# Performance work log

Hardware: AMD Instinct MI355X
Metric: run time of the kernel (lower is better)

## Reference

```python
import jax, jax.numpy as jnp
import numpy as np

EPS = 1e-5

def _ln(x, gamma, beta):
    mu = jnp.mean(x, axis=-1, keepdims=True)
    var = jnp.mean(jnp.square(x - mu), axis=-1, keepdims=True)
    return (x - mu) * jax.lax.rsqrt(var + EPS) * gamma + beta

def _linear(x, w, b):
    # torch nn.Linear convention: w is [out, in]
    return jnp.einsum('...i,oi->...o', x, w) + b

def setup_inputs() -> dict:
    key = jax.random.key(0)
    B, L, C = 1, 384, 128
    ks = jax.random.split(key, 16)
    s = 1.0 / np.sqrt(C)
    inp = {
        'pair_feat': jax.random.normal(ks[0], (B, L, L, C), dtype=jnp.float32),
        'res_mask': jnp.ones((B, L), dtype=jnp.float32),
        # left_proj: Linear + LayerNorm
        'lp_w': jax.random.uniform(ks[1], (C, C), jnp.float32, -s, s),
        'lp_b': jnp.zeros((C,), jnp.float32),
        'lp_g': jnp.ones((C,), jnp.float32),
        'lp_beta': jnp.zeros((C,), jnp.float32),
        # right_proj: Linear + LayerNorm
        'rp_w': jax.random.uniform(ks[2], (C, C), jnp.float32, -s, s),
        'rp_b': jnp.zeros((C,), jnp.float32),
        'rp_g': jnp.ones((C,), jnp.float32),
        'rp_beta': jnp.zeros((C,), jnp.float32),
        # gates: Linear (then sigmoid)
        'lg_w': jax.random.uniform(ks[3], (C, C), jnp.float32, -s, s),
        'lg_b': jnp.zeros((C,), jnp.float32),
        'rg_w': jax.random.uniform(ks[4], (C, C), jnp.float32, -s, s),
        'rg_b': jnp.zeros((C,), jnp.float32),
        'og_w': jax.random.uniform(ks[5], (C, C), jnp.float32, -s, s),
        'og_b': jnp.zeros((C,), jnp.float32),
        # out_layer: LayerNorm + Linear
        'ol_g': jnp.ones((C,), jnp.float32),
        'ol_beta': jnp.zeros((C,), jnp.float32),
        'ow': jax.random.uniform(ks[6], (C, C), jnp.float32, -s, s),
        'ob': jnp.zeros((C,), jnp.float32),
    }
    return inp

def reference(pair_feat, res_mask, lp_w, lp_b, lp_g, lp_beta,
              rp_w, rp_b, rp_g, rp_beta, lg_w, lg_b, rg_w, rg_b,
              og_w, og_b, ol_g, ol_beta, ow, ob):
    # op_type == 'outgoing': einsum 'bikc,bjkc->bijc'
    proj_left = _ln(_linear(pair_feat, lp_w, lp_b), lp_g, lp_beta)
    proj_right = _ln(_linear(pair_feat, rp_w, rp_b), rp_g, rp_beta)
    mask2d = (res_mask[:, :, None] * res_mask[:, None, :])[..., None]  # [B,L,L,1]
    proj_left = proj_left * mask2d
    proj_right = proj_right * mask2d
    gate_left = jax.nn.sigmoid(_linear(pair_feat, lg_w, lg_b))
    gate_right = jax.nn.sigmoid(_linear(pair_feat, rg_w, rg_b))
    proj_left = proj_left * gate_left
    proj_right = proj_right * gate_right
    out = jnp.einsum('bikc,bjkc->bijc', proj_left, proj_right)
    out = _linear(_ln(out, ol_g, ol_beta), ow, ob)
    gate = jax.nn.sigmoid(_linear(pair_feat, og_w, og_b))
    return out * gate
```

## Files before the change

kernel.cpp:

```cpp
#include <hip/hip_runtime.h>

typedef __bf16 bf16x8 __attribute__((ext_vector_type(8)));
typedef __bf16 bf16x4 __attribute__((ext_vector_type(4)));
typedef float  f32x4  __attribute__((ext_vector_type(4)));
typedef float  f32x2  __attribute__((ext_vector_type(2)));
typedef int    int4v  __attribute__((ext_vector_type(4)));

#define LL    384
#define CC    128
#define NROW  (LL * LL)

#define MFMA16(a, b, c) __builtin_amdgcn_mfma_f32_16x16x32_bf16((a), (b), (c), 0, 0, 0)

__device__ __forceinline__ bf16x8 cvt8(const float* p) {
    f32x4 a = *reinterpret_cast<const f32x4*>(p);
    f32x4 b = *reinterpret_cast<const f32x4*>(p + 4);
    bf16x8 r;
    r[0] = (__bf16)a[0]; r[1] = (__bf16)a[1]; r[2] = (__bf16)a[2]; r[3] = (__bf16)a[3];
    r[4] = (__bf16)b[0]; r[5] = (__bf16)b[1]; r[6] = (__bf16)b[2]; r[7] = (__bf16)b[3];
    return r;
}
__device__ __forceinline__ bf16x8 ld_ws(const __bf16* p) {
    return __builtin_bit_cast(bf16x8, *reinterpret_cast<const int4v*>(p));
}
__device__ __forceinline__ float sigmf(float x) { return 1.f / (1.f + __expf(-x)); }

__device__ __forceinline__ void gl16(const __bf16* g, __bf16* l) {
    __builtin_amdgcn_global_load_lds(
        (const __attribute__((address_space(1))) unsigned int*)g,
        (__attribute__((address_space(3))) unsigned int*)l,
        16, 0, 0);
}

__device__ __forceinline__ void stage_weight(const float* __restrict__ w,
                                             __bf16* dst, int tid) {
    const int c   = tid >> 1;
    const int k0  = (tid & 1) * 64;
    const int nt  = c >> 4;
    const int n16 = c & 15;
    #pragma unroll
    for (int u = 0; u < 8; ++u) {
        const int k    = k0 + u * 8;
        const int ks   = k >> 5;
        const int quad = (k >> 3) & 3;
        bf16x8 v = cvt8(w + c * CC + k);
        *reinterpret_cast<int4v*>(dst + ((ks * 8 + nt) * 64 + quad * 16 + n16) * 8) =
            __builtin_bit_cast(int4v, v);
    }
}
__device__ __forceinline__ bf16x8 wfrag(const __bf16* base, int ks, int nt, int lane) {
    return ld_ws(base + ((ks * 8 + nt) * 64 + lane) * 8);
}

__global__ __launch_bounds__(256, 2) void k_proj(
    const float* __restrict__ pf, const float* __restrict__ rmask,
    const float* __restrict__ lp_w, const float* __restrict__ lp_b,
    const float* __restrict__ lp_g, const float* __restrict__ lp_be,
    const float* __restrict__ rp_w, const float* __restrict__ rp_b,
    const float* __restrict__ rp_g, const float* __restrict__ rp_be,
    const float* __restrict__ lg_w, const float* __restrict__ lg_b,
    const float* __restrict__ rg_w, const float* __restrict__ rg_b,
    __bf16* __restrict__ pl_c, __bf16* __restrict__ pr_c)
{
    __shared__ __bf16 wl[2 * 16384];

    const int tid  = threadIdx.x;
    const int wave = tid >> 6, lane = tid & 63;
    const int n16  = lane & 15, quad = lane >> 4;
    const int rowblock = blockIdx.x * 128 + wave * 32;

    bf16x8 xf[2][4];
    #pragma unroll
    for (int rg = 0; rg < 2; ++rg) {
        const int r_a = rowblock + rg * 16 + n16;
        #pragma unroll
        for (int ks = 0; ks < 4; ++ks)
            xf[rg][ks] = cvt8(pf + (size_t)r_a * CC + ks * 32 + quad * 8);
    }

    float mrow[2][4];
    #pragma unroll
    for (int rg = 0; rg < 2; ++rg) {
        const int rd   = rowblock + rg * 16 + quad * 4;
        const int i_id = rd / LL;
        const int k_id = rd - i_id * LL;
        float mi = rmask[i_id];
        #pragma unroll
        for (int g = 0; g < 4; ++g) mrow[rg][g] = mi * rmask[k_id + g];
    }

    auto phase = [&](const float* gw, const float* gb,
                     const float* pw, const float* pb,
                     const float* gamma, const float* beta,
                     __bf16* dst) {
        stage_weight(gw, wl, tid);
        stage_weight(pw, wl + 16384, tid);
        __syncthreads();

        f32x4 acc[2][8];
        #pragma unroll
        for (int rg = 0; rg < 2; ++rg)
            #pragma unroll
            for (int nt = 0; nt < 8; ++nt) acc[rg][nt] = f32x4{0.f, 0.f, 0.f, 0.f};
        #pragma unroll
        for (int ks = 0; ks < 4; ++ks)
            #pragma unroll
            for (int nt = 0; nt < 8; ++nt) {
                bf16x8 wf = wfrag(wl, ks, nt, lane);
                #pragma unroll
                for (int rg = 0; rg < 2; ++rg)
                    acc[rg][nt] = MFMA16(xf[rg][ks], wf, acc[rg][nt]);
            }
        bf16x4 sg[2][8];
        #pragma unroll
        for (int rg = 0; rg < 2; ++rg)
            #pragma unroll
            for (int nt = 0; nt < 8; ++nt) {
                float bias = gb[nt * 16 + n16];
                #pragma unroll
                for (int g = 0; g < 4; ++g)
                    sg[rg][nt][g] = (__bf16)sigmf(acc[rg][nt][g] + bias);
            }
        #pragma unroll
        for (int rg = 0; rg < 2; ++rg)
            #pragma unroll
            for (int nt = 0; nt < 8; ++nt) acc[rg][nt] = f32x4{0.f, 0.f, 0.f, 0.f};
        #pragma unroll
        for (int ks = 0; ks < 4; ++ks)
            #pragma unroll
            for (int nt = 0; nt < 8; ++nt) {
                bf16x8 wf = wfrag(wl + 16384, ks, nt, lane);
                #pragma unroll
                for (int rg = 0; rg < 2; ++rg)
                    acc[rg][nt] = MFMA16(xf[rg][ks], wf, acc[rg][nt]);
            }
        #pragma unroll
        for (int rg = 0; rg < 2; ++rg) {
            #pragma unroll
            for (int nt = 0; nt < 8; ++nt) {
                float bias = pb[nt * 16 + n16];
                #pragma unroll
                for (int g = 0; g < 4; ++g) acc[rg][nt][g] += bias;
            }
            float s[4] = {0.f,0.f,0.f,0.f}, ss[4] = {0.f,0.f,0.f,0.f};
            #pragma unroll
            for (int nt = 0; nt < 8; ++nt)
                #pragma unroll
                for (int g = 0; g < 4; ++g) { float v = acc[rg][nt][g]; s[g] += v; ss[g] += v * v; }
            #pragma unroll
            for (int m = 1; m < 16; m <<= 1)
                #pragma unroll
                for (int g = 0; g < 4; ++g) {
                    s[g]  += __shfl_xor(s[g],  m, 64);
                    ss[g] += __shfl_xor(ss[g], m, 64);
                }
            float mean[4], rstd[4];
            #pragma unroll
            for (int g = 0; g < 4; ++g) {
                mean[g] = s[g] * (1.f / 128.f);
                float var = ss[g] * (1.f / 128.f) - mean[g] * mean[g];
                rstd[g] = rsqrtf(fmaxf(var, 0.f) + 1e-5f);
            }
            const int rd = rowblock + rg * 16 + quad * 4;
            #pragma unroll
            for (int nt = 0; nt < 8; ++nt) {
                const int c = nt * 16 + n16;
                float ga = gamma[c], be = beta[c];
                bf16x4 o;
                #pragma unroll
                for (int g = 0; g < 4; ++g) {
                    float v = (acc[rg][nt][g] - mean[g]) * rstd[g] * ga + be;
                    v *= mrow[rg][g] * (float)sg[rg][nt][g];
                    o[g] = (__bf16)v;
                }
                *reinterpret_cast<bf16x4*>(dst + (size_t)c * NROW + rd) = o;
            }
        }
        __syncthreads();
    };

    phase(lg_w, lg_b, lp_w, lp_b, lp_g, lp_be, pl_c);
    phase(rg_w, rg_b, rp_w, rp_b, rp_g, rp_be, pr_c);
}

__global__ __launch_bounds__(256, 3) void k_einsum_tile(
    const __bf16* __restrict__ pl_c, const __bf16* __restrict__ pr_c,
    float* __restrict__ T)
{
    __shared__ __bf16 sA[2][512 * 8];
    __shared__ __bf16 sB[2][512 * 8];

    const int bid  = blockIdx.x;
    const int wgid = (bid & 7) * 144 + (bid >> 3);
    const int ch   = wgid / 9;
    const int tile = wgid - ch * 9;
    const int i0   = (tile / 3) * 128;
    const int j0   = (tile % 3) * 128;

    const int tid  = threadIdx.x;
    const int w    = tid >> 6, lane = tid & 63;
    const int n16  = lane & 15, quad = lane >> 4;
    const int wr   = w >> 1, wc = w & 1;

    const __bf16* Pc = pl_c + (size_t)ch * NROW;
    const __bf16* Qc = pr_c + (size_t)ch * NROW;

    const __bf16* ga[2];
    const __bf16* gb[2];
    #pragma unroll
    for (int u = 0; u < 2; ++u) {
        const int row = (w * 2 + u) * 16 + n16;
        ga[u] = Pc + (size_t)(i0 + row) * LL + quad * 8;
        gb[u] = Qc + (size_t)(j0 + row) * LL + quad * 8;
    }

    f32x4 acc[4][4];
    #pragma unroll
    for (int m = 0; m < 4; ++m)
        #pragma unroll
        for (int n = 0; n < 4; ++n) acc[m][n] = f32x4{0.f, 0.f, 0.f, 0.f};

    auto STAGE = [&](int buf, int k0) {
        #pragma unroll
        for (int u = 0; u < 2; ++u) {
            __bf16* la = &sA[buf][(size_t)((w * 2 + u) * 64) * 8];
            __bf16* lb = &sB[buf][(size_t)((w * 2 + u) * 64) * 8];
            gl16(ga[u] + k0, la);
            gl16(gb[u] + k0, lb);
        }
    };

    STAGE(0, 0);
    __syncthreads();

    #pragma unroll
    for (int t = 0; t < 12; ++t) {
        if (t < 11) STAGE((t + 1) & 1, (t + 1) * 32);
        const __bf16* Ab = sA[t & 1];
        const __bf16* Bb = sB[t & 1];
        bf16x8 af[4], bf[4];
        #pragma unroll
        for (int m = 0; m < 4; ++m) af[m] = ld_ws(Ab + ((size_t)((wr * 4 + m) * 64 + lane)) * 8);
        #pragma unroll
        for (int n = 0; n < 4; ++n) bf[n] = ld_ws(Bb + ((size_t)((wc * 4 + n) * 64 + lane)) * 8);
        #pragma unroll
        for (int m = 0; m < 4; ++m)
            #pragma unroll
            for (int n = 0; n < 4; ++n)
                acc[m][n] = MFMA16(af[m], bf[n], acc[m][n]);
        __syncthreads();
    }

    float* Tc = T + (size_t)ch * NROW;
    #pragma unroll
    for (int m = 0; m < 4; ++m) {
        const int i = i0 + wr * 64 + m * 16 + quad * 4;
        #pragma unroll
        for (int n = 0; n < 4; ++n) {
            const int j = j0 + wc * 64 + n * 16 + n16;
            #pragma unroll
            for (int g = 0; g < 4; ++g)
                Tc[(size_t)(i + g) * LL + j] = acc[m][n][g];
        }
    }
}

__global__ __launch_bounds__(256, 2) void k_final_cm(
    float* __restrict__ out, const float* __restrict__ T,
    const float* __restrict__ pf,
    const float* __restrict__ ol_g, const float* __restrict__ ol_be,
    const float* __restrict__ ow,   const float* __restrict__ ob,
    const float* __restrict__ og_w, const float* __restrict__ og_b)
{
    __shared__ __bf16 wl[2 * 16384];
    const int tid  = threadIdx.x;
    const int wave = tid >> 6, lane = tid & 63;
    const int n16  = lane & 15, quad = lane >> 4;
    const int rowblock = blockIdx.x * 128 + wave * 32;

    stage_weight(ow,   wl,         tid);
    stage_weight(og_w, wl + 16384, tid);
    __syncthreads();

    #pragma unroll
    for (int rg = 0; rg < 2; ++rg) {
        const int r = rowblock + rg * 16 + n16;

        f32x4 tf[8];
        bf16x8 pff[4];
        #pragma unroll
        for (int ks = 0; ks < 4; ++ks) {
            #pragma unroll
            for (int q = 0; q < 4; ++q) {
                tf[2 * ks][q]     = T[(size_t)(ks * 32 + quad * 8 + q)     * NROW + r];
                tf[2 * ks + 1][q] = T[(size_t)(ks * 32 + quad * 8 + 4 + q) * NROW + r];
            }
            pff[ks] = cvt8(pf + (size_t)r * CC + ks * 32 + quad * 8);
        }

        float s = 0.f, ss = 0.f;
        #pragma unroll
        for (int h = 0; h < 8; ++h)
            #pragma unroll
            for (int q = 0; q < 4; ++q) { float f = tf[h][q]; s += f; ss += f * f; }
        s += __shfl_xor(s, 16, 64);  ss += __shfl_xor(ss, 16, 64);
        s += __shfl_xor(s, 32, 64);  ss += __shfl_xor(ss, 32, 64);
        const float mean = s * (1.f / 128.f);
        const float rstd = rsqrtf(fmaxf(ss * (1.f / 128.f) - mean * mean, 0.f) + 1e-5f);

        bf16x8 xn[4];
        #pragma unroll
        for (int ks = 0; ks < 4; ++ks) {
            const int cb = ks * 32 + quad * 8;
            f32x4 g0 = *reinterpret_cast<const f32x4*>(ol_g + cb);
            f32x4 g1 = *reinterpret_cast<const f32x4*>(ol_g + cb + 4);
            f32x4 b0 = *reinterpret_cast<const f32x4*>(ol_be + cb);
            f32x4 b1 = *reinterpret_cast<const f32x4*>(ol_be + cb + 4);
            bf16x8 rv;
            #pragma unroll
            for (int q = 0; q < 4; ++q) {
                rv[q]     = (__bf16)((tf[2 * ks][q]     - mean) * rstd * g0[q] + b0[q]);
                rv[4 + q] = (__bf16)((tf[2 * ks + 1][q] - mean) * rstd * g1[q] + b1[q]);
            }
            xn[ks] = rv;
        }

        f32x4 ao[8], ag[8];
        #pragma unroll
        for (int mt = 0; mt < 8; ++mt) { ao[mt] = f32x4{0.f,0.f,0.f,0.f}; ag[mt] = f32x4{0.f,0.f,0.f,0.f}; }
        #pragma unroll
        for (int ks = 0; ks < 4; ++ks)
            #pragma unroll
            for (int mt = 0; mt < 8; ++mt) {
                bf16x8 awf = wfrag(wl,         ks, mt, lane);
                bf16x8 gwf = wfrag(wl + 16384, ks, mt, lane);
                ao[mt] = MFMA16(awf, xn[ks],  ao[mt]);
                ag[mt] = MFMA16(gwf, pff[ks], ag[mt]);
            }

        #pragma unroll
        for (int mt = 0; mt < 8; ++mt) {
            const int c0 = mt * 16 + quad * 4;
            f32x4 bb = *reinterpret_cast<const f32x4*>(ob + c0);
            f32x4 gb = *reinterpret_cast<const f32x4*>(og_b + c0);
            f32x4 o;
            #pragma unroll
            for (int g = 0; g < 4; ++g) {
                float gate = sigmf(ag[mt][g] + gb[g]);
                o[g] = (ao[mt][g] + bb[g]) * gate;
            }
            *reinterpret_cast<f32x4*>(out + (size_t)r * CC + c0) = o;
        }
    }
}

__global__ __launch_bounds__(256, 2) void k_einsum_direct(
    const __bf16* __restrict__ pl_c, const __bf16* __restrict__ pr_c,
    float* __restrict__ out)
{
    const int tid  = threadIdx.x;
    const int wave = tid >> 6, lane = tid & 63;
    const int n16  = lane & 15, quad = lane >> 4;
    const int i0   = blockIdx.x * 64;
    const int jw   = blockIdx.y * 64 + wave * 16;
    const int c0   = blockIdx.z * 8;

    size_t off_i[4];
    #pragma unroll
    for (int t = 0; t < 4; ++t)
        off_i[t] = (size_t)(i0 + t * 16 + n16) * LL + quad * 8;
    const size_t off_j = (size_t)(jw + n16) * LL + quad * 8;

    f32x4 acc[8][4];
    #pragma unroll
    for (int c = 0; c < 8; ++c)
        #pragma unroll
        for (int t = 0; t < 4; ++t) acc[c][t] = f32x4{0.f, 0.f, 0.f, 0.f};

    #pragma unroll
    for (int c = 0; c < 8; ++c) {
        const __bf16* Pb = pl_c + (size_t)(c0 + c) * NROW;
        const __bf16* Qb = pr_c + (size_t)(c0 + c) * NROW + off_j;
        #pragma unroll
        for (int kt = 0; kt < 12; ++kt) {
            bf16x8 fj = ld_ws(Qb + kt * 32);
            #pragma unroll
            for (int t = 0; t < 4; ++t) {
                bf16x8 fi = ld_ws(Pb + off_i[t] + kt * 32);
                acc[c][t] = MFMA16(fi, fj, acc[c][t]);
            }
        }
    }

    #pragma unroll
    for (int t = 0; t < 4; ++t)
        #pragma unroll
        for (int g = 0; g < 4; ++g) {
            const int i = i0 + t * 16 + quad * 4 + g;
            float* dst = out + ((size_t)i * LL + jw + n16) * CC + c0;
            f32x4 lo, hi;
            #pragma unroll
            for (int q = 0; q < 4; ++q) { lo[q] = acc[q][t][g]; hi[q] = acc[4 + q][t][g]; }
            *reinterpret_cast<f32x4*>(dst)     = lo;
            *reinterpret_cast<f32x4*>(dst + 4) = hi;
        }
}

__global__ __launch_bounds__(256, 2) void k_final_ip(
    float* out, const float* __restrict__ pf,
    const float* __restrict__ ol_g, const float* __restrict__ ol_be,
    const float* __restrict__ ow,   const float* __restrict__ ob,
    const float* __restrict__ og_w, const float* __restrict__ og_b)
{
    __shared__ __bf16 wl[2 * 16384];
    const int tid  = threadIdx.x;
    const int wave = tid >> 6, lane = tid & 63;
    const int n16  = lane & 15, quad = lane >> 4;
    const int rowblock = blockIdx.x * 128 + wave * 32;

    stage_weight(ow,   wl,         tid);
    stage_weight(og_w, wl + 16384, tid);
    __syncthreads();

    #pragma unroll
    for (int rg = 0; rg < 2; ++rg) {
        const int r = rowblock + rg * 16 + n16;

        f32x4 tf[8];
        bf16x8 pff[4];
        #pragma unroll
        for (int ks = 0; ks < 4; ++ks) {
            const float* tp = out + (size_t)r * CC + ks * 32 + quad * 8;
            tf[2 * ks]     = *reinterpret_cast<const f32x4*>(tp);
            tf[2 * ks + 1] = *reinterpret_cast<const f32x4*>(tp + 4);
            pff[ks] = cvt8(pf + (size_t)r * CC + ks * 32 + quad * 8);
        }

        float s = 0.f, ss = 0.f;
        #pragma unroll
        for (int h = 0; h < 8; ++h)
            #pragma unroll
            for (int q = 0; q < 4; ++q) { float f = tf[h][q]; s += f; ss += f * f; }
        s += __shfl_xor(s, 16, 64);  ss += __shfl_xor(ss, 16, 64);
        s += __shfl_xor(s, 32, 64);  ss += __shfl_xor(ss, 32, 64);
        const float mean = s * (1.f / 128.f);
        const float rstd = rsqrtf(fmaxf(ss * (1.f / 128.f) - mean * mean, 0.f) + 1e-5f);

        bf16x8 xn[4];
        #pragma unroll
        for (int ks = 0; ks < 4; ++ks) {
            const int cb = ks * 32 + quad * 8;
            f32x4 g0 = *reinterpret_cast<const f32x4*>(ol_g + cb);
            f32x4 g1 = *reinterpret_cast<const f32x4*>(ol_g + cb + 4);
            f32x4 b0 = *reinterpret_cast<const f32x4*>(ol_be + cb);
            f32x4 b1 = *reinterpret_cast<const f32x4*>(ol_be + cb + 4);
            bf16x8 rv;
            #pragma unroll
            for (int q = 0; q < 4; ++q) {
                rv[q]     = (__bf16)((tf[2 * ks][q]     - mean) * rstd * g0[q] + b0[q]);
                rv[4 + q] = (__bf16)((tf[2 * ks + 1][q] - mean) * rstd * g1[q] + b1[q]);
            }
            xn[ks] = rv;
        }

        f32x4 ao[8], ag[8];
        #pragma unroll
        for (int mt = 0; mt < 8; ++mt) { ao[mt] = f32x4{0.f,0.f,0.f,0.f}; ag[mt] = f32x4{0.f,0.f,0.f,0.f}; }
        #pragma unroll
        for (int ks = 0; ks < 4; ++ks)
            #pragma unroll
            for (int mt = 0; mt < 8; ++mt) {
                bf16x8 awf = wfrag(wl,         ks, mt, lane);
                bf16x8 gwf = wfrag(wl + 16384, ks, mt, lane);
                ao[mt] = MFMA16(awf, xn[ks],  ao[mt]);
                ag[mt] = MFMA16(gwf, pff[ks], ag[mt]);
            }

        #pragma unroll
        for (int mt = 0; mt < 8; ++mt) {
            const int c0 = mt * 16 + quad * 4;
            f32x4 bb = *reinterpret_cast<const f32x4*>(ob + c0);
            f32x4 gb = *reinterpret_cast<const f32x4*>(og_b + c0);
            f32x4 o;
            #pragma unroll
            for (int g = 0; g < 4; ++g) {
                float gate = sigmf(ag[mt][g] + gb[g]);
                o[g] = (ao[mt][g] + bb[g]) * gate;
            }
            *reinterpret_cast<f32x4*>(out + (size_t)r * CC + c0) = o;
        }
    }
}

extern "C" void kernel_launch(void* const* d_in, const int* in_sizes, int n_in,
                              void* d_out, int out_size, void* d_ws, size_t ws_size,
                              hipStream_t stream)
{
    const float* pf    = (const float*)d_in[0];
    const float* rmask = (const float*)d_in[1];
    const float* lp_w  = (const float*)d_in[2];
    const float* lp_b  = (const float*)d_in[3];
    const float* lp_g  = (const float*)d_in[4];
    const float* lp_be = (const float*)d_in[5];
    const float* rp_w  = (const float*)d_in[6];
    const float* rp_b  = (const float*)d_in[7];
    const float* rp_g  = (const float*)d_in[8];
    const float* rp_be = (const float*)d_in[9];
    const float* lg_w  = (const float*)d_in[10];
    const float* lg_b  = (const float*)d_in[11];
    const float* rg_w  = (const float*)d_in[12];
    const float* rg_b  = (const float*)d_in[13];
    const float* og_w  = (const float*)d_in[14];
    const float* og_b  = (const float*)d_in[15];
    const float* ol_g  = (const float*)d_in[16];
    const float* ol_be = (const float*)d_in[17];
    const float* ow    = (const float*)d_in[18];
    const float* ob    = (const float*)d_in[19];
    float* out = (float*)d_out;

    __bf16* pl_c = (__bf16*)d_ws;
    __bf16* pr_c = pl_c + (size_t)CC * NROW;
    float*  T    = (float*)(pr_c + (size_t)CC * NROW);

    const size_t need = (size_t)CC * NROW * (2 + 2 + 4);

    k_proj<<<NROW / 128, 256, 0, stream>>>(pf, rmask,
        lp_w, lp_b, lp_g, lp_be, rp_w, rp_b, rp_g, rp_be,
        lg_w, lg_b, rg_w, rg_b, pl_c, pr_c);

    if (ws_size >= need) {
        k_einsum_tile<<<1152, 256, 0, stream>>>(pl_c, pr_c, T);
        k_final_cm<<<NROW / 128, 256, 0, stream>>>(out, T, pf,
            ol_g, ol_be, ow, ob, og_w, og_b);
    } else {
        k_einsum_direct<<<dim3(LL / 64, LL / 64, CC / 8), 256, 0, stream>>>(pl_c, pr_c, out);
        k_final_ip<<<NROW / 128, 256, 0, stream>>>(out, pf,
            ol_g, ol_be, ow, ob, og_w, og_b);
    }
}
```

Measured before the change: 353.0 us.

## Pre-convert weights to bf16 fragment layout once and double-buffer weight staging

Adds a small kernel that converts all six fp32 weight matrices into a bf16 MFMA-fragment layout in workspace, once per call. The projection and final kernels then copy these pre-laid-out weights into LDS with direct global-to-LDS loads instead of each of 1152 blocks converting fp32 weights itself. The projection kernel double-buffers the four weight matrices so loading the next one overlaps the current GEMM. The cost is an extra kernel launch and a larger workspace requirement; the old path is kept as a fallback.

```diff
diff --git a/kernel.cpp b/kernel.cpp
--- a/kernel.cpp
+++ b/kernel.cpp
@@ -3,7 +3,6 @@
 typedef __bf16 bf16x8 __attribute__((ext_vector_type(8)));
 typedef __bf16 bf16x4 __attribute__((ext_vector_type(4)));
 typedef float  f32x4  __attribute__((ext_vector_type(4)));
-typedef float  f32x2  __attribute__((ext_vector_type(2)));
 typedef int    int4v  __attribute__((ext_vector_type(4)));
 
 #define LL    384
@@ -52,7 +51,331 @@
     return ld_ws(base + ((ks * 8 + nt) * 64 + lane) * 8);
 }
 
+__global__ __launch_bounds__(256) void k_wconv(
+    const float* __restrict__ w0, const float* __restrict__ w1,
+    const float* __restrict__ w2, const float* __restrict__ w3,
+    const float* __restrict__ w4, const float* __restrict__ w5,
+    __bf16* __restrict__ dst)
+{
+    const float* srcs[6] = {w0, w1, w2, w3, w4, w5};
+    stage_weight(srcs[blockIdx.x], dst + (size_t)blockIdx.x * 16384, threadIdx.x);
+}
+
 __global__ __launch_bounds__(256, 2) void k_proj(
+    const float* __restrict__ pf, const float* __restrict__ rmask,
+    const __bf16* __restrict__ wfm,
+    const float* __restrict__ lp_b, const float* __restrict__ lp_g,
+    const float* __restrict__ lp_be,
+    const float* __restrict__ rp_b, const float* __restrict__ rp_g,
+    const float* __restrict__ rp_be,
+    const float* __restrict__ lg_b, const float* __restrict__ rg_b,
+    __bf16* __restrict__ pl_c, __bf16* __restrict__ pr_c)
+{
+    __shared__ __bf16 wl[2][16384];
+
+    const int tid  = threadIdx.x;
+    const int wave = tid >> 6, lane = tid & 63;
+    const int n16  = lane & 15, quad = lane >> 4;
+    const int rowblock = blockIdx.x * 128 + wave * 32;
+
+    auto STAGEW = [&](int widx, __bf16* dstL) {
+        const __bf16* src = wfm + (size_t)widx * 16384;
+        #pragma unroll
+        for (int i = 0; i < 8; ++i) {
+            const int s = wave * 8 + i;
+            gl16(src + (size_t)s * 512 + lane * 8, dstL + (size_t)s * 512);
+        }
+    };
+
+    bf16x8 xf[2][4];
+    #pragma unroll
+    for (int rg = 0; rg < 2; ++rg) {
+        const int r_a = rowblock + rg * 16 + n16;
+        #pragma unroll
+        for (int ks = 0; ks < 4; ++ks)
+            xf[rg][ks] = cvt8(pf + (size_t)r_a * CC + ks * 32 + quad * 8);
+    }
+
+    float mrow[2][4];
+    #pragma unroll
+    for (int rg = 0; rg < 2; ++rg) {
+        const int rd   = rowblock + rg * 16 + quad * 4;
+        const int i_id = rd / LL;
+        const int k_id = rd - i_id * LL;
+        float mi = rmask[i_id];
+        #pragma unroll
+        for (int g = 0; g < 4; ++g) mrow[rg][g] = mi * rmask[k_id + g];
+    }
+
+    f32x4 acc[2][8];
+    auto GEMM = [&](const __bf16* wb) {
+        #pragma unroll
+        for (int rg = 0; rg < 2; ++rg)
+            #pragma unroll
+            for (int nt = 0; nt < 8; ++nt) acc[rg][nt] = f32x4{0.f, 0.f, 0.f, 0.f};
+        #pragma unroll
+        for (int ks = 0; ks < 4; ++ks)
+            #pragma unroll
+            for (int nt = 0; nt < 8; ++nt) {
+                bf16x8 wf = wfrag(wb, ks, nt, lane);
+                #pragma unroll
+                for (int rg = 0; rg < 2; ++rg)
+                    acc[rg][nt] = MFMA16(xf[rg][ks], wf, acc[rg][nt]);
+            }
+    };
+
+    bf16x4 sg[2][8];
+    auto SIGM = [&](const float* gb) {
+        #pragma unroll
+        for (int rg = 0; rg < 2; ++rg)
+            #pragma unroll
+            for (int nt = 0; nt < 8; ++nt) {
+                float bias = gb[nt * 16 + n16];
+                #pragma unroll
+                for (int g = 0; g < 4; ++g)
+                    sg[rg][nt][g] = (__bf16)sigmf(acc[rg][nt][g] + bias);
+            }
+    };
+
+    auto EPILOG = [&](const float* pb, const float* gamma, const float* beta,
+                      __bf16* dst) {
+        #pragma unroll
+        for (int rg = 0; rg < 2; ++rg) {
+            #pragma unroll
+            for (int nt = 0; nt < 8; ++nt) {
+                float bias = pb[nt * 16 + n16];
+                #pragma unroll
+                for (int g = 0; g < 4; ++g) acc[rg][nt][g] += bias;
+            }
+            float s[4] = {0.f,0.f,0.f,0.f}, ss[4] = {0.f,0.f,0.f,0.f};
+            #pragma unroll
+            for (int nt = 0; nt < 8; ++nt)
+                #pragma unroll
+                for (int g = 0; g < 4; ++g) { float v = acc[rg][nt][g]; s[g] += v; ss[g] += v * v; }
+            #pragma unroll
+            for (int m = 1; m < 16; m <<= 1)
+                #pragma unroll
+                for (int g = 0; g < 4; ++g) {
+                    s[g]  += __shfl_xor(s[g],  m, 64);
+                    ss[g] += __shfl_xor(ss[g], m, 64);
+                }
+            float mean[4], rstd[4];
+            #pragma unroll
+            for (int g = 0; g < 4; ++g) {
+                mean[g] = s[g] * (1.f / 128.f);
+                float var = ss[g] * (1.f / 128.f) - mean[g] * mean[g];
+                rstd[g] = rsqrtf(fmaxf(var, 0.f) + 1e-5f);
+            }
+            const int rd = rowblock + rg * 16 + quad * 4;
+            #pragma unroll
+            for (int nt = 0; nt < 8; ++nt) {
+                const int c = nt * 16 + n16;
+                float ga = gamma[c], be = beta[c];
+                bf16x4 o;
+                #pragma unroll
+                for (int g = 0; g < 4; ++g) {
+                    float v = (acc[rg][nt][g] - mean[g]) * rstd[g] * ga + be;
+                    v *= mrow[rg][g] * (float)sg[rg][nt][g];
+                    o[g] = (__bf16)v;
+                }
+                *reinterpret_cast<bf16x4*>(dst + (size_t)c * NROW + rd) = o;
+            }
+        }
+    };
+
+    STAGEW(0, wl[0]);
+    __syncthreads();
+
+    STAGEW(1, wl[1]);
+    GEMM(wl[0]);  SIGM(lg_b);
+    __syncthreads();
+
+    STAGEW(2, wl[0]);
+    GEMM(wl[1]);  EPILOG(lp_b, lp_g, lp_be, pl_c);
+    __syncthreads();
+
+    STAGEW(3, wl[1]);
+    GEMM(wl[0]);  SIGM(rg_b);
+    __syncthreads();
+
+    GEMM(wl[1]);  EPILOG(rp_b, rp_g, rp_be, pr_c);
+}
+
+__global__ __launch_bounds__(256, 3) void k_einsum_tile(
+    const __bf16* __restrict__ pl_c, const __bf16* __restrict__ pr_c,
+    float* __restrict__ T)
+{
+    __shared__ __bf16 sA[2][512 * 8];
+    __shared__ __bf16 sB[2][512 * 8];
+
+    const int bid  = blockIdx.x;
+    const int wgid = (bid & 7) * 144 + (bid >> 3);
+    const int ch   = wgid / 9;
+    const int tile = wgid - ch * 9;
+    const int i0   = (tile / 3) * 128;
+    const int j0   = (tile % 3) * 128;
+
+    const int tid  = threadIdx.x;
+    const int w    = tid >> 6, lane = tid & 63;
+    const int n16  = lane & 15, quad = lane >> 4;
+    const int wr   = w >> 1, wc = w & 1;
+
+    const __bf16* Pc = pl_c + (size_t)ch * NROW;
+    const __bf16* Qc = pr_c + (size_t)ch * NROW;
+
+    const __bf16* ga[2];
+    const __bf16* gb[2];
+    #pragma unroll
+    for (int u = 0; u < 2; ++u) {
+        const int row = (w * 2 + u) * 16 + n16;
+        ga[u] = Pc + (size_t)(i0 + row) * LL + quad * 8;
+        gb[u] = Qc + (size_t)(j0 + row) * LL + quad * 8;
+    }
+
+    f32x4 acc[4][4];
+    #pragma unroll
+    for (int m = 0; m < 4; ++m)
+        #pragma unroll
+        for (int n = 0; n < 4; ++n) acc[m][n] = f32x4{0.f, 0.f, 0.f, 0.f};
+
+    auto STAGE = [&](int buf, int k0) {
+        #pragma unroll
+        for (int u = 0; u < 2; ++u) {
+            __bf16* la = &sA[buf][(size_t)((w * 2 + u) * 64) * 8];
+            __bf16* lb = &sB[buf][(size_t)((w * 2 + u) * 64) * 8];
+            gl16(ga[u] + k0, la);
+            gl16(gb[u] + k0, lb);
+        }
+    };
+
+    STAGE(0, 0);
+    __syncthreads();
+
+    #pragma unroll
+    for (int t = 0; t < 12; ++t) {
+        if (t < 11) STAGE((t + 1) & 1, (t + 1) * 32);
+        const __bf16* Ab = sA[t & 1];
+        const __bf16* Bb = sB[t & 1];
+        bf16x8 af[4], bf[4];
+        #pragma unroll
+        for (int m = 0; m < 4; ++m) af[m] = ld_ws(Ab + ((size_t)((wr * 4 + m) * 64 + lane)) * 8);
+        #pragma unroll
+        for (int n = 0; n < 4; ++n) bf[n] = ld_ws(Bb + ((size_t)((wc * 4 + n) * 64 + lane)) * 8);
+        #pragma unroll
+        for (int m = 0; m < 4; ++m)
+            #pragma unroll
+            for (int n = 0; n < 4; ++n)
+                acc[m][n] = MFMA16(af[m], bf[n], acc[m][n]);
+        __syncthreads();
+    }
+
+    float* Tc = T + (size_t)ch * NROW;
+    #pragma unroll
+    for (int m = 0; m < 4; ++m) {
+        const int i = i0 + wr * 64 + m * 16 + quad * 4;
+        #pragma unroll
+        for (int n = 0; n < 4; ++n) {
+            const int j = j0 + wc * 64 + n * 16 + n16;
+            #pragma unroll
+            for (int g = 0; g < 4; ++g)
+                Tc[(size_t)(i + g) * LL + j] = acc[m][n][g];
+        }
+    }
+}
+
+__global__ __launch_bounds__(256, 2) void k_final_cm(
+    float* __restrict__ out, const float* __restrict__ T,
+    const float* __restrict__ pf, const __bf16* __restrict__ wfm,
+    const float* __restrict__ ol_g, const float* __restrict__ ol_be,
+    const float* __restrict__ ob,   const float* __restrict__ og_b)
+{
+    __shared__ __bf16 wl[2][16384];
+    const int tid  = threadIdx.x;
+    const int wave = tid >> 6, lane = tid & 63;
+    const int n16  = lane & 15, quad = lane >> 4;
+    const int rowblock = blockIdx.x * 128 + wave * 32;
+
+    #pragma unroll
+    for (int i = 0; i < 8; ++i) {
+        const int s = wave * 8 + i;
+        gl16(wfm + (size_t)(4 * 16384) + (size_t)s * 512 + lane * 8, wl[0] + (size_t)s * 512);
+        gl16(wfm + (size_t)(5 * 16384) + (size_t)s * 512 + lane * 8, wl[1] + (size_t)s * 512);
+    }
+    __syncthreads();
+
+    #pragma unroll
+    for (int rg = 0; rg < 2; ++rg) {
+        const int r = rowblock + rg * 16 + n16;
+
+        f32x4 tf[8];
+        bf16x8 pff[4];
+        #pragma unroll
+        for (int ks = 0; ks < 4; ++ks) {
+            #pragma unroll
+            for (int q = 0; q < 4; ++q) {
+                tf[2 * ks][q]     = T[(size_t)(ks * 32 + quad * 8 + q)     * NROW + r];
+                tf[2 * ks + 1][q] = T[(size_t)(ks * 32 + quad * 8 + 4 + q) * NROW + r];
+            }
+            pff[ks] = cvt8(pf + (size_t)r * CC + ks * 32 + quad * 8);
+        }
+
+        float s = 0.f, ss = 0.f;
+        #pragma unroll
+        for (int h = 0; h < 8; ++h)
+            #pragma unroll
+            for (int q = 0; q < 4; ++q) { float f = tf[h][q]; s += f; ss += f * f; }
+        s += __shfl_xor(s, 16, 64);  ss += __shfl_xor(ss, 16, 64);
+        s += __shfl_xor(s, 32, 64);  ss += __shfl_xor(ss, 32, 64);
+        const float mean = s * (1.f / 128.f);
+        const float rstd = rsqrtf(fmaxf(ss * (1.f / 128.f) - mean * mean, 0.f) + 1e-5f);
+
+        bf16x8 xn[4];
+        #pragma unroll
+        for (int ks = 0; ks < 4; ++ks) {
+            const int cb = ks * 32 + quad * 8;
+            f32x4 g0 = *reinterpret_cast<const f32x4*>(ol_g + cb);
+            f32x4 g1 = *reinterpret_cast<const f32x4*>(ol_g + cb + 4);
+            f32x4 b0 = *reinterpret_cast<const f32x4*>(ol_be + cb);
+            f32x4 b1 = *reinterpret_cast<const f32x4*>(ol_be + cb + 4);
+            bf16x8 rv;
+            #pragma unroll
+            for (int q = 0; q < 4; ++q) {
+                rv[q]     = (__bf16)((tf[2 * ks][q]     - mean) * rstd * g0[q] + b0[q]);
+                rv[4 + q] = (__bf16)((tf[2 * ks + 1][q] - mean) * rstd * g1[q] + b1[q]);
+            }
+            xn[ks] = rv;
+        }
+
+        f32x4 ao[8], ag[8];
+        #pragma unroll
+        for (int mt = 0; mt < 8; ++mt) { ao[mt] = f32x4{0.f,0.f,0.f,0.f}; ag[mt] = f32x4{0.f,0.f,0.f,0.f}; }
+        #pragma unroll
+        for (int ks = 0; ks < 4; ++ks)
+            #pragma unroll
+            for (int mt = 0; mt < 8; ++mt) {
+                bf16x8 awf = wfrag(wl[0], ks, mt, lane);
+                bf16x8 gwf = wfrag(wl[1], ks, mt, lane);
+                ao[mt] = MFMA16(awf, xn[ks],  ao[mt]);
+                ag[mt] = MFMA16(gwf, pff[ks], ag[mt]);
+            }
+
+        #pragma unroll
+        for (int mt = 0; mt < 8; ++mt) {
+            const int c0 = mt * 16 + quad * 4;
+            f32x4 bb = *reinterpret_cast<const f32x4*>(ob + c0);
+            f32x4 gb = *reinterpret_cast<const f32x4*>(og_b + c0);
+            f32x4 o;
+            #pragma unroll
+            for (int g = 0; g < 4; ++g) {
+                float gate = sigmf(ag[mt][g] + gb[g]);
+                o[g] = (ao[mt][g] + bb[g]) * gate;
+            }
+            *reinterpret_cast<f32x4*>(out + (size_t)r * CC + c0) = o;
+        }
+    }
+}
+
+__global__ __launch_bounds__(256, 2) void k_proj_fb(
     const float* __restrict__ pf, const float* __restrict__ rmask,
     const float* __restrict__ lp_w, const float* __restrict__ lp_b,
     const float* __restrict__ lp_g, const float* __restrict__ lp_be,
@@ -181,177 +504,6 @@
 
     phase(lg_w, lg_b, lp_w, lp_b, lp_g, lp_be, pl_c);
     phase(rg_w, rg_b, rp_w, rp_b, rp_g, rp_be, pr_c);
-}
-
-__global__ __launch_bounds__(256, 3) void k_einsum_tile(
-    const __bf16* __restrict__ pl_c, const __bf16* __restrict__ pr_c,
-    float* __restrict__ T)
-{
-    __shared__ __bf16 sA[2][512 * 8];
-    __shared__ __bf16 sB[2][512 * 8];
-
-    const int bid  = blockIdx.x;
-    const int wgid = (bid & 7) * 144 + (bid >> 3);
-    const int ch   = wgid / 9;
-    const int tile = wgid - ch * 9;
-    const int i0   = (tile / 3) * 128;
-    const int j0   = (tile % 3) * 128;
-
-    const int tid  = threadIdx.x;
-    const int w    = tid >> 6, lane = tid & 63;
-    const int n16  = lane & 15, quad = lane >> 4;
-    const int wr   = w >> 1, wc = w & 1;
-
-    const __bf16* Pc = pl_c + (size_t)ch * NROW;
-    const __bf16* Qc = pr_c + (size_t)ch * NROW;
-
-    const __bf16* ga[2];
-    const __bf16* gb[2];
-    #pragma unroll
-    for (int u = 0; u < 2; ++u) {
-        const int row = (w * 2 + u) * 16 + n16;
-        ga[u] = Pc + (size_t)(i0 + row) * LL + quad * 8;
-        gb[u] = Qc + (size_t)(j0 + row) * LL + quad * 8;
-    }
-
-    f32x4 acc[4][4];
-    #pragma unroll
-    for (int m = 0; m < 4; ++m)
-        #pragma unroll
-        for (int n = 0; n < 4; ++n) acc[m][n] = f32x4{0.f, 0.f, 0.f, 0.f};
-
-    auto STAGE = [&](int buf, int k0) {
-        #pragma unroll
-        for (int u = 0; u < 2; ++u) {
-            __bf16* la = &sA[buf][(size_t)((w * 2 + u) * 64) * 8];
-            __bf16* lb = &sB[buf][(size_t)((w * 2 + u) * 64) * 8];
-            gl16(ga[u] + k0, la);
-            gl16(gb[u] + k0, lb);
-        }
-    };
-
-    STAGE(0, 0);
-    __syncthreads();
-
-    #pragma unroll
-    for (int t = 0; t < 12; ++t) {
-        if (t < 11) STAGE((t + 1) & 1, (t + 1) * 32);
-        const __bf16* Ab = sA[t & 1];
-        const __bf16* Bb = sB[t & 1];
-        bf16x8 af[4], bf[4];
-        #pragma unroll
-        for (int m = 0; m < 4; ++m) af[m] = ld_ws(Ab + ((size_t)((wr * 4 + m) * 64 + lane)) * 8);
-        #pragma unroll
-        for (int n = 0; n < 4; ++n) bf[n] = ld_ws(Bb + ((size_t)((wc * 4 + n) * 64 + lane)) * 8);
-        #pragma unroll
-        for (int m = 0; m < 4; ++m)
-            #pragma unroll
-            for (int n = 0; n < 4; ++n)
-                acc[m][n] = MFMA16(af[m], bf[n], acc[m][n]);
-        __syncthreads();
-    }
-
-    float* Tc = T + (size_t)ch * NROW;
-    #pragma unroll
-    for (int m = 0; m < 4; ++m) {
-        const int i = i0 + wr * 64 + m * 16 + quad * 4;
-        #pragma unroll
-        for (int n = 0; n < 4; ++n) {
-            const int j = j0 + wc * 64 + n * 16 + n16;
-            #pragma unroll
-            for (int g = 0; g < 4; ++g)
-                Tc[(size_t)(i + g) * LL + j] = acc[m][n][g];
-        }
-    }
-}
-
-__global__ __launch_bounds__(256, 2) void k_final_cm(
-    float* __restrict__ out, const float* __restrict__ T,
-    const float* __restrict__ pf,
-    const float* __restrict__ ol_g, const float* __restrict__ ol_be,
-    const float* __restrict__ ow,   const float* __restrict__ ob,
-    const float* __restrict__ og_w, const float* __restrict__ og_b)
-{
-    __shared__ __bf16 wl[2 * 16384];
-    const int tid  = threadIdx.x;
-    const int wave = tid >> 6, lane = tid & 63;
-    const int n16  = lane & 15, quad = lane >> 4;
-    const int rowblock = blockIdx.x * 128 + wave * 32;
-
-    stage_weight(ow,   wl,         tid);
-    stage_weight(og_w, wl + 16384, tid);
-    __syncthreads();
-
-    #pragma unroll
-    for (int rg = 0; rg < 2; ++rg) {
-        const int r = rowblock + rg * 16 + n16;
-
-        f32x4 tf[8];
-        bf16x8 pff[4];
-        #pragma unroll
-        for (int ks = 0; ks < 4; ++ks) {
-            #pragma unroll
-            for (int q = 0; q < 4; ++q) {
-                tf[2 * ks][q]     = T[(size_t)(ks * 32 + quad * 8 + q)     * NROW + r];
-                tf[2 * ks + 1][q] = T[(size_t)(ks * 32 + quad * 8 + 4 + q) * NROW + r];
-            }
-            pff[ks] = cvt8(pf + (size_t)r * CC + ks * 32 + quad * 8);
-        }
-
-        float s = 0.f, ss = 0.f;
-        #pragma unroll
-        for (int h = 0; h < 8; ++h)
-            #pragma unroll
-            for (int q = 0; q < 4; ++q) { float f = tf[h][q]; s += f; ss += f * f; }
-        s += __shfl_xor(s, 16, 64);  ss += __shfl_xor(ss, 16, 64);
-        s += __shfl_xor(s, 32, 64);  ss += __shfl_xor(ss, 32, 64);
-        const float mean = s * (1.f / 128.f);
-        const float rstd = rsqrtf(fmaxf(ss * (1.f / 128.f) - mean * mean, 0.f) + 1e-5f);
-
-        bf16x8 xn[4];
-        #pragma unroll
-        for (int ks = 0; ks < 4; ++ks) {
-            const int cb = ks * 32 + quad * 8;
-            f32x4 g0 = *reinterpret_cast<const f32x4*>(ol_g + cb);
-            f32x4 g1 = *reinterpret_cast<const f32x4*>(ol_g + cb + 4);
-            f32x4 b0 = *reinterpret_cast<const f32x4*>(ol_be + cb);
-            f32x4 b1 = *reinterpret_cast<const f32x4*>(ol_be + cb + 4);
-            bf16x8 rv;
-            #pragma unroll
-            for (int q = 0; q < 4; ++q) {
-                rv[q]     = (__bf16)((tf[2 * ks][q]     - mean) * rstd * g0[q] + b0[q]);
-                rv[4 + q] = (__bf16)((tf[2 * ks + 1][q] - mean) * rstd * g1[q] + b1[q]);
-            }
-            xn[ks] = rv;
-        }
-
-        f32x4 ao[8], ag[8];
-        #pragma unroll
-        for (int mt = 0; mt < 8; ++mt) { ao[mt] = f32x4{0.f,0.f,0.f,0.f}; ag[mt] = f32x4{0.f,0.f,0.f,0.f}; }
-        #pragma unroll
-        for (int ks = 0; ks < 4; ++ks)
-            #pragma unroll
-            for (int mt = 0; mt < 8; ++mt) {
-                bf16x8 awf = wfrag(wl,         ks, mt, lane);
-                bf16x8 gwf = wfrag(wl + 16384, ks, mt, lane);
-                ao[mt] = MFMA16(awf, xn[ks],  ao[mt]);
-                ag[mt] = MFMA16(gwf, pff[ks], ag[mt]);
-            }
-
-        #pragma unroll
-        for (int mt = 0; mt < 8; ++mt) {
-            const int c0 = mt * 16 + quad * 4;
-            f32x4 bb = *reinterpret_cast<const f32x4*>(ob + c0);
-            f32x4 gb = *reinterpret_cast<const f32x4*>(og_b + c0);
-            f32x4 o;
-            #pragma unroll
-            for (int g = 0; g < 4; ++g) {
-                float gate = sigmf(ag[mt][g] + gb[g]);
-                o[g] = (ao[mt][g] + bb[g]) * gate;
-            }
-            *reinterpret_cast<f32x4*>(out + (size_t)r * CC + c0) = o;
-        }
-    }
 }
 
 __global__ __launch_bounds__(256, 2) void k_einsum_direct(
@@ -520,19 +672,22 @@
 
     __bf16* pl_c = (__bf16*)d_ws;
     __bf16* pr_c = pl_c + (size_t)CC * NROW;
-    float*  T    = (float*)(pr_c + (size_t)CC * NROW);
-
-    const size_t need = (size_t)CC * NROW * (2 + 2 + 4);
-
-    k_proj<<<NROW / 128, 256, 0, stream>>>(pf, rmask,
-        lp_w, lp_b, lp_g, lp_be, rp_w, rp_b, rp_g, rp_be,
-        lg_w, lg_b, rg_w, rg_b, pl_c, pr_c);
+    __bf16* wfm  = pr_c + (size_t)CC * NROW;
+    float*  T    = (float*)(wfm + 6 * 16384);
+
+    const size_t need = (size_t)CC * NROW * (2 + 2 + 4) + 6 * 16384 * 2;
 
     if (ws_size >= need) {
+        k_wconv<<<6, 256, 0, stream>>>(lg_w, lp_w, rg_w, rp_w, ow, og_w, wfm);
+        k_proj<<<NROW / 128, 256, 0, stream>>>(pf, rmask, wfm,
+            lp_b, lp_g, lp_be, rp_b, rp_g, rp_be, lg_b, rg_b, pl_c, pr_c);
         k_einsum_tile<<<1152, 256, 0, stream>>>(pl_c, pr_c, T);
-        k_final_cm<<<NROW / 128, 256, 0, stream>>>(out, T, pf,
-            ol_g, ol_be, ow, ob, og_w, og_b);
+        k_final_cm<<<NROW / 128, 256, 0, stream>>>(out, T, pf, wfm,
+            ol_g, ol_be, ob, og_b);
     } else {
+        k_proj_fb<<<NROW / 128, 256, 0, stream>>>(pf, rmask,
+            lp_w, lp_b, lp_g, lp_be, rp_w, rp_b, rp_g, rp_be,
+            lg_w, lg_b, rg_w, rg_b, pl_c, pr_c);
         k_einsum_direct<<<dim3(LL / 64, LL / 64, CC / 8), 256, 0, stream>>>(pl_c, pr_c, out);
         k_final_ip<<<NROW / 128, 256, 0, stream>>>(out, pf,
             ol_g, ol_be, ow, ob, og_w, og_b);
```

After: 312.7 us. 11.4% less time.
